# Optimization experiments

Hardware: AMD Instinct MI355X
Metric: run time of the kernel (lower is better)

The kernel has to match this reference:

```python
import jax, jax.numpy as jnp
import numpy as np

B, NSP, H, W = 8, 1024, 256, 256   # frames, superpixels/frame, label-map size
N = B * NSP                        # total superpixel nodes
MIX = 0.5                          # mixing_coeff
SIGMA = 0.05


def _interp_axis(x, out, axis):
    # 1-D bilinear interpolation along `axis`, align_corners=True
    n = x.shape[axis]
    pos = jnp.linspace(0.0, n - 1.0, out).astype(x.dtype)
    i0 = jnp.floor(pos).astype(jnp.int32)
    i1 = jnp.minimum(i0 + 1, n - 1)
    wt = pos - i0.astype(x.dtype)
    shp = [1] * x.ndim
    shp[axis] = out
    wt = wt.reshape(shp)
    return jnp.take(x, i0, axis=axis) * (1 - wt) + jnp.take(x, i1, axis=axis) * wt


def _upsample_ac(x, oh, ow):
    # nn.UpsamplingBilinear2d (align_corners=True)
    if x.shape[2] == oh and x.shape[3] == ow:
        return x
    return _interp_axis(_interp_axis(x, oh, 2), ow, 3)


def _sp_pool(feats, seg):
    # upsample [B,C,h,w] to label resolution, then average features per superpixel -> [N, C]
    C = feats.shape[1]
    up = _upsample_ac(feats, H, W)
    vals = up.transpose(0, 2, 3, 1).reshape(-1, C)          # [B*H*W, C]
    sums = jax.ops.segment_sum(vals, seg, num_segments=N)
    cnt = jax.ops.segment_sum(jnp.ones((seg.shape[0],), vals.dtype), seg, num_segments=N)
    return sums / jnp.maximum(cnt, 1.0)[:, None]


def _gcn(x, Wm, b, src, dst, ew):
    # GCNConv(normalize=False): out_i = sum_{j->i} ew * (x_j @ W) + b
    h = x @ Wm
    agg = jax.ops.segment_sum(h[src] * ew[:, None], dst, num_segments=x.shape[0])
    return agg + b


def _coord_map():
    # channel 0 varies along dim2 (w), channel 1 varies along dim3 (h), both in [0,1]
    c0 = jnp.broadcast_to((jnp.arange(H, dtype=jnp.float32) / (H - 1))[:, None], (H, W))
    c1 = jnp.broadcast_to((jnp.arange(W, dtype=jnp.float32) / (W - 1))[None, :], (H, W))
    return jnp.broadcast_to(jnp.stack([c0, c1], 0)[None], (B, 2, H, W))


def setup_inputs() -> dict:
    key = jax.random.key(0)
    ks = jax.random.split(key, 12)
    labels = jax.random.randint(ks[0], (B, 1, H, W), 0, NSP, dtype=jnp.int32)
    skip0 = jax.random.normal(ks[1], (B, 512, 32, 32), jnp.float32)
    skip1 = jax.random.normal(ks[2], (B, 256, 64, 64), jnp.float32)
    skip2 = jax.random.normal(ks[3], (B, 256, 128, 128), jnp.float32)
    E = 131072
    edges_nn = jax.random.randint(ks[4], (2, E), 0, N, dtype=jnp.int32)
    negs = jax.random.randint(ks[5], (E,), 0, N, dtype=jnp.int32)
    W0 = jax.random.normal(ks[6], (512, 256), jnp.float32) / np.float32(np.sqrt(512))
    W1 = jax.random.normal(ks[7], (256, 256), jnp.float32) / np.float32(np.sqrt(256))
    W2 = jax.random.normal(ks[8], (256, 256), jnp.float32) / np.float32(np.sqrt(256))
    lin_w = jax.random.normal(ks[9], (256, 1), jnp.float32) / np.float32(np.sqrt(256))
    z = jnp.zeros((256,), jnp.float32)
    return {"labels": labels, "skip0": skip0, "skip1": skip1, "skip2": skip2,
            "edges_nn": edges_nn, "negs": negs,
            "W0": W0, "b0": z, "W1": W1, "b1": z, "W2": W2, "b2": z, "lin_w": lin_w}


def reference(labels, skip0, skip1, skip2, edges_nn, negs, W0, b0, W1, b1, W2, b2, lin_w):
    # per-pixel global superpixel id (offset per frame)
    seg = (labels.reshape(B, -1) + NSP * jnp.arange(B, dtype=labels.dtype)[:, None]).reshape(-1)
    src, dst = edges_nn[0], edges_nn[1]

    # pooled normalized coordinates per superpixel -> gaussian edge weights
    pc = _sp_pool(_coord_map(), seg)                        # [N, 2]
    dr = pc[src] - pc[dst]
    dist = jnp.linalg.norm(dr, axis=1)
    edge_attr = jnp.exp(-dist ** 2 / SIGMA)

    x = _sp_pool(skip0, seg)                                # [N, 512]
    layers = [(W0, b0, None), (W1, b1, skip1), (W2, b2, skip2)]
    for i, (Wm, b, sk) in enumerate(layers):
        if i > 0:
            x = (1 - MIX) * x + MIX * _sp_pool(sk, seg)
        x = jax.nn.relu(_gcn(x, Wm, b, src, dst, edge_attr))

    s = x @ lin_w                                           # [N, 1]
    dap = jax.nn.sigmoid(s[src] - s[dst])
    dan = jax.nn.sigmoid(s[src] - s[negs])
    return dan, dap, edge_attr
```

## Files before the change

### kernel.cpp

```cpp
#include <hip/hip_runtime.h>
#include <hip/hip_fp16.h>
#include <cstdint>
#include <cstddef>

#define BB 8
#define NSPX 1024
#define NNODE 8192
#define EE 131072
#define NPIX 524288
#define CH 256

typedef unsigned int uint;
typedef unsigned long long u64;

__device__ __forceinline__ uint packh2(float a, float b) {
  __half2 h = __float22half2_rn(make_float2(a, b));
  return *reinterpret_cast<uint*>(&h);
}
__device__ __forceinline__ __half2 uh2(uint u) { return *reinterpret_cast<__half2*>(&u); }
__device__ __forceinline__ uint h2u(__half2 h) { return *reinterpret_cast<uint*>(&h); }

__global__ __launch_bounds__(256) void zero_kernel(int4* p, int n4) {
  int i = blockIdx.x * 256 + threadIdx.x;
  int stride = gridDim.x * 256;
  int4 z = make_int4(0, 0, 0, 0);
  for (; i < n4; i += stride) p[i] = z;
}

__global__ __launch_bounds__(256) void cnt2_kernel(const int* __restrict__ labels,
                                                   const int* __restrict__ edst,
                                                   int* __restrict__ segb,
                                                   u64* __restrict__ packed,
                                                   int* __restrict__ cnt_e) {
  int blk = blockIdx.x;
  int t = threadIdx.x;
  if (blk < 2048) {
    int p = blk * 256 + t;
    int b = p >> 16;
    int h = (p >> 8) & 255;
    int w = p & 255;
    int seg = labels[p] + (b << 10);
    segb[p] = seg;
    u64 enc = (1ULL << 48) | ((u64)h << 24) | (u64)w;
    atomicAdd(&packed[seg], enc);
  } else {
    int e = (blk - 2048) * 256 + t;
    atomicAdd(&cnt_e[edst[e]], 1);
  }
}

__global__ __launch_bounds__(1024) void fusedB_kernel(const u64* __restrict__ packed,
                                                      const int* __restrict__ cnt_e,
                                                      int* __restrict__ poff, int* __restrict__ eoff,
                                                      float* __restrict__ rcnt,
                                                      float* __restrict__ pch, float* __restrict__ pcw) {
  int blk = blockIdx.x;
  int t = threadIdx.x;
  if (blk < 2) {
    __shared__ int ps[1024];
    int which = blk;
    int* coff = which ? eoff : poff;
    int base = t * 8;
    int v[8];
    int sum = 0;
#pragma unroll
    for (int i = 0; i < 8; ++i) {
      int x = which ? cnt_e[base + i] : (int)(packed[base + i] >> 48);
      v[i] = sum;
      sum += x;
    }
    ps[t] = sum;
    __syncthreads();
    for (int off = 1; off < 1024; off <<= 1) {
      int x = (t >= off) ? ps[t - off] : 0;
      __syncthreads();
      ps[t] += x;
      __syncthreads();
    }
    int prev = (t == 0) ? 0 : ps[t - 1];
#pragma unroll
    for (int i = 0; i < 8; ++i) coff[base + i] = prev + v[i];
    if (t == 1023) coff[8192] = ps[1023];
  } else {
    int n = (blk - 2) * 1024 + t;
    u64 v = packed[n];
    int c = (int)(v >> 48);
    int sh = (int)((v >> 24) & 0xFFFFFF);
    int sw = (int)(v & 0xFFFFFF);
    float r = 1.0f / (float)(c > 1 ? c : 1);
    rcnt[n] = r;
    pch[n] = (float)sh * r * (1.0f / 255.0f);
    pcw[n] = (float)sw * r * (1.0f / 255.0f);
  }
}

__device__ __forceinline__ void dev_transpose_h(const float* __restrict__ src, __half* __restrict__ dst,
                                                int C, int P, int b, int p0, int c0, int t,
                                                uint (*tile)[33]) {
  int l16 = t & 15, r16 = t >> 4;
#pragma unroll
  for (int pass = 0; pass < 4; ++pass) {
    int c = r16 + pass * 16;
    float4 v = *(const float4*)&src[((size_t)b * C + c0 + c) * P + p0 + l16 * 4];
    tile[c][l16 * 2]     = packh2(v.x, v.y);
    tile[c][l16 * 2 + 1] = packh2(v.z, v.w);
  }
  __syncthreads();
  int l8 = t & 7, r32 = t >> 3;
#pragma unroll
  for (int pass = 0; pass < 2; ++pass) {
    int p = r32 + pass * 32;
    int ph = p >> 1;
    int odd = p & 1;
    uint r[4];
#pragma unroll
    for (int q = 0; q < 4; ++q) {
      uint ua = tile[l8 * 8 + 2 * q][ph];
      uint ub = tile[l8 * 8 + 2 * q + 1][ph];
      r[q] = odd ? ((ua >> 16) | (ub & 0xFFFF0000u))
                 : ((ua & 0xFFFFu) | (ub << 16));
    }
    *(uint4*)&dst[((size_t)b * P + p0 + p) * C + c0 + l8 * 8] = make_uint4(r[0], r[1], r[2], r[3]);
  }
}

__device__ __forceinline__ void dev_gemm_kmaj(const float* __restrict__ A, const float* __restrict__ W,
                                              __half* __restrict__ out, int idx, int t,
                                              float (*As)[36]) {
  int b = idx >> 6;
  int m0 = (idx & 31) * 32;
  int n0 = ((idx >> 5) & 1) * 128;
  int ct = t & 31;
  int rm = t >> 5;
  int l8 = t & 7, kr = t >> 3;
  const float* Ab = A + (size_t)b * 512 * 1024;
  float4 acc[4];
#pragma unroll
  for (int i = 0; i < 4; ++i) acc[i] = make_float4(0.f, 0.f, 0.f, 0.f);
  for (int k0 = 0; k0 < 512; k0 += 64) {
#pragma unroll
    for (int pass = 0; pass < 2; ++pass) {
      int k = kr + pass * 32;
      float4 v = *(const float4*)&Ab[(size_t)(k0 + k) * 1024 + m0 + l8 * 4];
      *(float4*)&As[k][l8 * 4] = v;
    }
    __syncthreads();
#pragma unroll 8
    for (int k = 0; k < 64; ++k) {
      float4 a = *(const float4*)&As[k][rm * 4];
      float4 wv = *(const float4*)&W[(size_t)(k0 + k) * 256 + n0 + ct * 4];
      acc[0].x += a.x * wv.x; acc[0].y += a.x * wv.y; acc[0].z += a.x * wv.z; acc[0].w += a.x * wv.w;
      acc[1].x += a.y * wv.x; acc[1].y += a.y * wv.y; acc[1].z += a.y * wv.z; acc[1].w += a.y * wv.w;
      acc[2].x += a.z * wv.x; acc[2].y += a.z * wv.y; acc[2].z += a.z * wv.z; acc[2].w += a.z * wv.w;
      acc[3].x += a.w * wv.x; acc[3].y += a.w * wv.y; acc[3].z += a.w * wv.z; acc[3].w += a.w * wv.w;
    }
    __syncthreads();
  }
#pragma unroll
  for (int i = 0; i < 4; ++i) {
    int m = m0 + rm * 4 + i;
    uint2 pk = make_uint2(packh2(acc[i].x, acc[i].y), packh2(acc[i].z, acc[i].w));
    *(uint2*)&out[((size_t)b * 1024 + m) * 256 + n0 + ct * 4] = pk;
  }
}

__global__ __launch_bounds__(256) void fusedT_kernel(const float* __restrict__ skip1,
                                                     __half* __restrict__ F1t,
                                                     const float* __restrict__ skip2,
                                                     __half* __restrict__ F2t,
                                                     const float* __restrict__ skip0,
                                                     const float* __restrict__ W0,
                                                     __half* __restrict__ F0b,
                                                     const int* __restrict__ segb,
                                                     const int* __restrict__ poff,
                                                     int* __restrict__ pcur,
                                                     int* __restrict__ psorted,
                                                     const int* __restrict__ esrc,
                                                     const int* __restrict__ edst,
                                                     const float* __restrict__ pch,
                                                     const float* __restrict__ pcw,
                                                     const int* __restrict__ eoff,
                                                     int* __restrict__ ecur,
                                                     uint2* __restrict__ evw,
                                                     float* __restrict__ outp) {
  __shared__ __align__(16) char smem[9216];
  int blk = blockIdx.x;
  int t = threadIdx.x;
  if (blk >= 12800) {
    dev_gemm_kmaj(skip0, W0, F0b, blk - 12800, t, (float(*)[36])smem);
    return;
  }
  int s = blk % 5;
  int q = blk / 5;
  if (s < 4) {
    int idx = q * 4 + s;
    if (idx < 8192) {
      int p0 = (idx & 255) * 64;
      int c0 = ((idx >> 8) & 3) * 64;
      int b = idx >> 10;
      dev_transpose_h(skip2, F2t, 256, 16384, b, p0, c0, t, (uint(*)[33])smem);
    } else {
      int i2 = idx - 8192;
      int p0 = (i2 & 63) * 64;
      int c0 = ((i2 >> 6) & 3) * 64;
      int b = i2 >> 8;
      dev_transpose_h(skip1, F1t, 256, 4096, b, p0, c0, t, (uint(*)[33])smem);
    }
  } else {
    if (q < 2048) {
      int p = q * 256 + t;
      int sg = segb[p];
      int pos = poff[sg] + atomicAdd(&pcur[sg], 1);
      psorted[pos] = p;
    } else {
      int e = (q - 2048) * 256 + t;
      int s1 = esrc[e], d1 = edst[e];
      float dh = pch[s1] - pch[d1];
      float dw = pcw[s1] - pcw[d1];
      float ea = expf(-(dh * dh + dw * dw) * 20.0f);
      outp[2 * EE + e] = ea;
      int pos = eoff[d1] + atomicAdd(&ecur[d1], 1);
      evw[pos] = make_uint2((uint)s1, __float_as_uint(ea));
    }
  }
}

__device__ __forceinline__ void tap16(const __half* __restrict__ tp, float wt, __half2* acc) {
  uint4 qa = *(const uint4*)tp;
  uint4 qb = *(const uint4*)(tp + 8);
  __half2 W = __float2half2_rn(wt);
  acc[0] = __hfma2(W, uh2(qa.x), acc[0]);
  acc[1] = __hfma2(W, uh2(qa.y), acc[1]);
  acc[2] = __hfma2(W, uh2(qa.z), acc[2]);
  acc[3] = __hfma2(W, uh2(qa.w), acc[3]);
  acc[4] = __hfma2(W, uh2(qb.x), acc[4]);
  acc[5] = __hfma2(W, uh2(qb.y), acc[5]);
  acc[6] = __hfma2(W, uh2(qb.z), acc[6]);
  acc[7] = __hfma2(W, uh2(qb.w), acc[7]);
}

template <int HS>
__device__ __forceinline__ void taps16(const __half* __restrict__ fb, int h, int w, __half2* acc) {
  const float fh = (float)(HS - 1) / 255.0f;
  float ph = h * fh, pw = w * fh;
  int i0 = (int)ph, j0 = (int)pw;
  float th = ph - (float)i0, tw = pw - (float)j0;
  int i1 = min(i0 + 1, HS - 1), jj1 = min(j0 + 1, HS - 1);
  float w11 = th * tw, w10 = th - w11, w01 = tw - w11, w00 = 1.f - th - tw + w11;
  tap16(fb + (i0 * HS + j0) * 256, w00, acc);
  tap16(fb + (i0 * HS + jj1) * 256, w01, acc);
  tap16(fb + (i1 * HS + j0) * 256, w10, acc);
  tap16(fb + (i1 * HS + jj1) * 256, w11, acc);
}

__global__ __launch_bounds__(256) void fusedC_kernel(const __half* __restrict__ F0,
                                                     const __half* __restrict__ F1,
                                                     const __half* __restrict__ F2,
                                                     const int* __restrict__ poff,
                                                     const int* __restrict__ psorted,
                                                     const float* __restrict__ rc,
                                                     __half* __restrict__ p0out,
                                                     float* __restrict__ p1out,
                                                     float* __restrict__ p2out) {
  __shared__ __align__(16) char smem[18432];
  int blk = blockIdx.x;
  int t = threadIdx.x;
  if (blk >= 8192 && blk < 16384) {
    int x = blk - 8192;
    int n = ((x & 7) << 10) | (x >> 3);
    int b = n >> 10;
    int l = t & 15;
    int s = t >> 4;
    const __half* f0 = F0 + (size_t)b * 1024 * 256 + l * 16;
    const __half* f1 = F1 + (size_t)b * 4096 * 256 + l * 16;
    int j1 = poff[n + 1];
    __half2 z = __float2half2_rn(0.f);
    __half2 a0[8], a1[8];
#pragma unroll
    for (int i = 0; i < 8; ++i) { a0[i] = z; a1[i] = z; }
    for (int j = poff[n] + s; j < j1; j += 16) {
      int p = psorted[j];
      int h = (p >> 8) & 255, w = p & 255;
      taps16<32>(f0, h, w, a0);
      taps16<64>(f1, h, w, a1);
    }
    uint (*red)[256][9] = (uint(*)[256][9])smem;
#pragma unroll
    for (int k = 0; k < 8; ++k) { red[0][t][k] = h2u(a0[k]); red[1][t][k] = h2u(a1[k]); }
    __syncthreads();
    if (t < 128) {
      int l2 = t >> 3, k = t & 7;
      float r = rc[n];
      float2 s0 = make_float2(0.f, 0.f), s1 = s0;
#pragma unroll
      for (int ss = 0; ss < 16; ++ss) {
        float2 v0 = __half22float2(uh2(red[0][ss * 16 + l2][k]));
        float2 v1 = __half22float2(uh2(red[1][ss * 16 + l2][k]));
        s0.x += v0.x; s0.y += v0.y;
        s1.x += v1.x; s1.y += v1.y;
      }
      int c = l2 * 16 + k * 2;
      *(uint*)&p0out[(size_t)n * 256 + c] = packh2(s0.x * r, s0.y * r);
      *(float2*)&p1out[(size_t)n * 256 + c] = make_float2(s1.x * r, s1.y * r);
    }
  } else {
    int x, c0;
    if (blk < 8192) { x = blk; c0 = 0; }
    else            { x = blk - 16384; c0 = 128; }
    int n = ((x & 7) << 10) | (x >> 3);
    int b = n >> 10;
    int l = t & 7;
    int s = t >> 3;
    const __half* fb = F2 + (size_t)b * 16384 * 256 + c0 + l * 16;
    int j1 = poff[n + 1];
    __half2 z = __float2half2_rn(0.f);
    __half2 acc[8];
#pragma unroll
    for (int i = 0; i < 8; ++i) acc[i] = z;
    for (int j = poff[n] + s; j < j1; j += 32) {
      int p = psorted[j];
      int h = (p >> 8) & 255, w = p & 255;
      taps16<128>(fb, h, w, acc);
    }
    uint (*red)[9] = (uint(*)[9])smem;
#pragma unroll
    for (int k = 0; k < 8; ++k) red[t][k] = h2u(acc[k]);
    __syncthreads();
    if (t < 64) {
      int l2 = t >> 3, k = t & 7;
      float r = rc[n];
      float2 sm = make_float2(0.f, 0.f);
#pragma unroll
      for (int ss = 0; ss < 32; ++ss) {
        float2 v = __half22float2(uh2(red[ss * 8 + l2][k]));
        sm.x += v.x; sm.y += v.y;
      }
      int c = c0 + l2 * 16 + k * 2;
      *(float2*)&p2out[(size_t)n * 256 + c] = make_float2(sm.x * r, sm.y * r);
    }
  }
}

__global__ __launch_bounds__(256) void agg_kernel(const __half* __restrict__ h, const float* __restrict__ bias,
                                                  const int* __restrict__ eoff,
                                                  const uint2* __restrict__ evw,
                                                  float* __restrict__ xout) {
  int n = blockIdx.x * 2 + (threadIdx.x >> 7);
  int c2 = threadIdx.x & 127;
  int e0 = eoff[n], e1 = eoff[n + 1];
  float a0 = 0.f, a1 = 0.f;
  for (int j = e0; j < e1; ++j) {
    uint2 ev = evw[j];
    float wv = __uint_as_float(ev.y);
    uint hv = *(const uint*)&h[((size_t)ev.x << 8) + c2 * 2];
    float2 f = __half22float2(uh2(hv));
    a0 += wv * f.x;
    a1 += wv * f.y;
  }
  float v0 = a0 + bias[2 * c2];
  float v1 = a1 + bias[2 * c2 + 1];
  *(float2*)&xout[((size_t)n << 8) + 2 * c2] =
      make_float2(v0 > 0.f ? v0 : 0.f, v1 > 0.f ? v1 : 0.f);
}

__global__ __launch_bounds__(256) void agg_score_kernel(const __half* __restrict__ h,
                                                        const float* __restrict__ bias,
                                                        const int* __restrict__ eoff,
                                                        const uint2* __restrict__ evw,
                                                        const float* __restrict__ lw,
                                                        float* __restrict__ s) {
  int t = threadIdx.x;
  int n = blockIdx.x * 2 + (t >> 7);
  int c2 = t & 127;
  int e0 = eoff[n], e1 = eoff[n + 1];
  float a0 = 0.f, a1 = 0.f;
  for (int j = e0; j < e1; ++j) {
    uint2 ev = evw[j];
    float wv = __uint_as_float(ev.y);
    uint hv = *(const uint*)&h[((size_t)ev.x << 8) + c2 * 2];
    float2 f = __half22float2(uh2(hv));
    a0 += wv * f.x;
    a1 += wv * f.y;
  }
  float v0 = a0 + bias[2 * c2];
  float v1 = a1 + bias[2 * c2 + 1];
  v0 = v0 > 0.f ? v0 : 0.f;
  v1 = v1 > 0.f ? v1 : 0.f;
  float p = v0 * lw[2 * c2] + v1 * lw[2 * c2 + 1];
#pragma unroll
  for (int off = 32; off > 0; off >>= 1) p += __shfl_down(p, off, 64);
  __shared__ float ws[4];
  if ((t & 63) == 0) ws[t >> 6] = p;
  __syncthreads();
  if (t == 0)   s[n] = ws[0] + ws[1];
  if (t == 128) s[n] = ws[2] + ws[3];
}

__global__ __launch_bounds__(256) void gemm_mix_n256(const float* __restrict__ X, const float* __restrict__ Pl,
                                                     const float* __restrict__ W, __half* __restrict__ out) {
  const int t = threadIdx.x;
  const int r0 = blockIdx.x * 16;
  const int cw = (t & 63) * 4;
  const int rg = (t >> 6) * 4;
  __shared__ float Xl[16][68];
  float4 acc[4];
#pragma unroll
  for (int i = 0; i < 4; ++i) acc[i] = make_float4(0.f, 0.f, 0.f, 0.f);
  for (int k0 = 0; k0 < 256; k0 += 64) {
#pragma unroll
    for (int l = 0; l < 4; ++l) {
      int idx = t + 256 * l;
      int r = idx >> 6, k = idx & 63;
      size_t a = (size_t)(r0 + r) * 256 + k0 + k;
      Xl[r][k] = 0.5f * (X[a] + Pl[a]);
    }
    __syncthreads();
#pragma unroll
    for (int k4 = 0; k4 < 64; k4 += 4) {
      float4 a[4];
#pragma unroll
      for (int i = 0; i < 4; ++i) a[i] = *(const float4*)&Xl[rg + i][k4];
#pragma unroll
      for (int kk = 0; kk < 4; ++kk) {
        float4 w = *(const float4*)&W[(size_t)(k0 + k4 + kk) * 256 + cw];
#pragma unroll
        for (int i = 0; i < 4; ++i) {
          float av = ((const float*)&a[i])[kk];
          acc[i].x += av * w.x;
          acc[i].y += av * w.y;
          acc[i].z += av * w.z;
          acc[i].w += av * w.w;
        }
      }
    }
    __syncthreads();
  }
#pragma unroll
  for (int i = 0; i < 4; ++i) {
    uint2 pk = make_uint2(packh2(acc[i].x, acc[i].y), packh2(acc[i].z, acc[i].w));
    *(uint2*)&out[(size_t)(r0 + rg + i) * 256 + cw] = pk;
  }
}

__global__ __launch_bounds__(256) void out_kernel(const float* __restrict__ s, const int* __restrict__ src,
                                                  const int* __restrict__ dst, const int* __restrict__ negs,
                                                  float* __restrict__ outp) {
  int e = blockIdx.x * 256 + threadIdx.x;
  if (e >= EE) return;
  float ss = s[src[e]];
  float a = ss - s[negs[e]];
  float b = ss - s[dst[e]];
  outp[e] = 1.0f / (1.0f + expf(-a));
  outp[EE + e] = 1.0f / (1.0f + expf(-b));
}

extern "C" void kernel_launch(void* const* d_in, const int* in_sizes, int n_in,
                              void* d_out, int out_size, void* d_ws, size_t ws_size,
                              hipStream_t stream) {
  const int*   labels = (const int*)d_in[0];
  const float* skip0  = (const float*)d_in[1];
  const float* skip1  = (const float*)d_in[2];
  const float* skip2  = (const float*)d_in[3];
  const int*   edges  = (const int*)d_in[4];
  const int*   negs   = (const int*)d_in[5];
  const float* W0     = (const float*)d_in[6];
  const float* b0     = (const float*)d_in[7];
  const float* W1     = (const float*)d_in[8];
  const float* b1     = (const float*)d_in[9];
  const float* W2     = (const float*)d_in[10];
  const float* b2     = (const float*)d_in[11];
  const float* lw     = (const float*)d_in[12];
  const int* esrc = edges;
  const int* edst = edges + EE;
  float* outp = (float*)d_out;

  size_t o = 0;
  char* base = (char*)d_ws;
  auto alloc = [&](size_t bytes) -> void* {
    void* p = base + o;
    o += (bytes + 255) & ~(size_t)255;
    return p;
  };
  u64* packed  = (u64*)alloc(NNODE * 8);
  int* cnt_e   = (int*)alloc(NNODE * 4);
  int* ecur    = (int*)alloc(NNODE * 4);
  int* pcur    = (int*)alloc(NNODE * 4);
  size_t zbytes = o;
  float*  rcnt    = (float*)alloc(NNODE * 4);
  float*  pch     = (float*)alloc(NNODE * 4);
  float*  pcw     = (float*)alloc(NNODE * 4);
  int*    poff    = (int*)alloc((NNODE + 1) * 4);
  int*    eoff    = (int*)alloc((NNODE + 1) * 4);
  uint2*  evw     = (uint2*)alloc((size_t)EE * 8);
  int*    psorted = (int*)alloc(NPIX * 4);
  int*    segb    = (int*)alloc(NPIX * 4);
  float*  bufA    = (float*)alloc((size_t)NNODE * CH * 4);
  float*  bufB    = (float*)alloc((size_t)NNODE * CH * 4);
  float*  p1buf   = (float*)alloc((size_t)NNODE * CH * 4);
  float*  p2buf   = (float*)alloc((size_t)NNODE * CH * 4);
  __half* h0b     = (__half*)alloc((size_t)NNODE * CH * 2);
  __half* h1b     = (__half*)alloc((size_t)NNODE * CH * 2);
  __half* F0b     = (__half*)alloc((size_t)BB * 1024 * CH * 2);
  __half* F1t     = (__half*)alloc((size_t)BB * 4096 * CH * 2);
  __half* F2t     = (__half*)alloc((size_t)BB * 16384 * CH * 2);
  float*  sbuf    = (float*)alloc(NNODE * 4);
  (void)ws_size; (void)n_in; (void)in_sizes; (void)out_size;

  zero_kernel<<<64, 256, 0, stream>>>((int4*)d_ws, (int)(zbytes / 16));
  cnt2_kernel<<<2048 + 512, 256, 0, stream>>>(labels, edst, segb, packed, cnt_e);
  fusedB_kernel<<<10, 1024, 0, stream>>>(packed, cnt_e, poff, eoff, rcnt, pch, pcw);
  fusedT_kernel<<<13312, 256, 0, stream>>>(skip1, F1t, skip2, F2t, skip0, W0, F0b,
                                           segb, poff, pcur, psorted,
                                           esrc, edst, pch, pcw, eoff, ecur, evw, outp);
  fusedC_kernel<<<24576, 256, 0, stream>>>(F0b, F1t, F2t, poff, psorted, rcnt,
                                           h0b, p1buf, p2buf);
  agg_kernel<<<NNODE / 2, 256, 0, stream>>>(h0b, b0, eoff, evw, bufB);
  gemm_mix_n256<<<NNODE / 16, 256, 0, stream>>>(bufB, p1buf, W1, h1b);
  agg_kernel<<<NNODE / 2, 256, 0, stream>>>(h1b, b1, eoff, evw, bufA);
  gemm_mix_n256<<<NNODE / 16, 256, 0, stream>>>(bufA, p2buf, W2, h1b);
  agg_score_kernel<<<NNODE / 2, 256, 0, stream>>>(h1b, b2, eoff, evw, lw, sbuf);
  out_kernel<<<EE / 256, 256, 0, stream>>>(sbuf, esrc, edst, negs, outp);
}
```

Before: 691.5 us.

## Split transposes into dedicated kernel with 256-pixel tiles, separate scatter/gemm kernel

```diff
diff --git a/kernel.cpp b/kernel.cpp
--- a/kernel.cpp
+++ b/kernel.cpp
@@ -94,21 +94,21 @@
   }
 }
 
-__device__ __forceinline__ void dev_transpose_h(const float* __restrict__ src, __half* __restrict__ dst,
-                                                int C, int P, int b, int p0, int c0, int t,
-                                                uint (*tile)[33]) {
-  int l16 = t & 15, r16 = t >> 4;
-#pragma unroll
-  for (int pass = 0; pass < 4; ++pass) {
-    int c = r16 + pass * 16;
-    float4 v = *(const float4*)&src[((size_t)b * C + c0 + c) * P + p0 + l16 * 4];
-    tile[c][l16 * 2]     = packh2(v.x, v.y);
-    tile[c][l16 * 2 + 1] = packh2(v.z, v.w);
+__device__ __forceinline__ void dev_transpose256(const float* __restrict__ src, __half* __restrict__ dst,
+                                                 int C, int P, int b, int p0, int c0, int t,
+                                                 uint (*tile)[129]) {
+  int l64 = t & 63, rch = t >> 6;
+#pragma unroll
+  for (int pass = 0; pass < 16; ++pass) {
+    int c = rch + pass * 4;
+    float4 v = *(const float4*)&src[((size_t)b * C + c0 + c) * P + p0 + l64 * 4];
+    tile[c][l64 * 2]     = packh2(v.x, v.y);
+    tile[c][l64 * 2 + 1] = packh2(v.z, v.w);
   }
   __syncthreads();
   int l8 = t & 7, r32 = t >> 3;
 #pragma unroll
-  for (int pass = 0; pass < 2; ++pass) {
+  for (int pass = 0; pass < 8; ++pass) {
     int p = r32 + pass * 32;
     int ph = p >> 1;
     int odd = p & 1;
@@ -121,6 +121,25 @@
                  : ((ua & 0xFFFFu) | (ub << 16));
     }
     *(uint4*)&dst[((size_t)b * P + p0 + p) * C + c0 + l8 * 8] = make_uint4(r[0], r[1], r[2], r[3]);
+  }
+}
+
+__global__ __launch_bounds__(256) void t2k_kernel(const float* __restrict__ skip2, __half* __restrict__ F2t,
+                                                  const float* __restrict__ skip1, __half* __restrict__ F1t) {
+  __shared__ uint tile[64][129];
+  int idx = blockIdx.x;
+  int t = threadIdx.x;
+  if (idx < 2048) {
+    int p0 = (idx & 63) * 256;
+    int c0 = ((idx >> 6) & 3) * 64;
+    int b = idx >> 8;
+    dev_transpose256(skip2, F2t, 256, 16384, b, p0, c0, t, tile);
+  } else {
+    int i2 = idx - 2048;
+    int p0 = (i2 & 15) * 256;
+    int c0 = ((i2 >> 4) & 3) * 64;
+    int b = i2 >> 6;
+    dev_transpose256(skip1, F1t, 256, 4096, b, p0, c0, t, tile);
   }
 }
 
@@ -164,11 +183,7 @@
   }
 }
 
-__global__ __launch_bounds__(256) void fusedT_kernel(const float* __restrict__ skip1,
-                                                     __half* __restrict__ F1t,
-                                                     const float* __restrict__ skip2,
-                                                     __half* __restrict__ F2t,
-                                                     const float* __restrict__ skip0,
+__global__ __launch_bounds__(256) void fusedS_kernel(const float* __restrict__ skip0,
                                                      const float* __restrict__ W0,
                                                      __half* __restrict__ F0b,
                                                      const int* __restrict__ segb,
@@ -183,45 +198,27 @@
                                                      int* __restrict__ ecur,
                                                      uint2* __restrict__ evw,
                                                      float* __restrict__ outp) {
-  __shared__ __align__(16) char smem[9216];
+  __shared__ __align__(16) float As[64][36];
   int blk = blockIdx.x;
   int t = threadIdx.x;
-  if (blk >= 12800) {
-    dev_gemm_kmaj(skip0, W0, F0b, blk - 12800, t, (float(*)[36])smem);
+  if (blk >= 2560) {
+    dev_gemm_kmaj(skip0, W0, F0b, blk - 2560, t, As);
     return;
   }
-  int s = blk % 5;
-  int q = blk / 5;
-  if (s < 4) {
-    int idx = q * 4 + s;
-    if (idx < 8192) {
-      int p0 = (idx & 255) * 64;
-      int c0 = ((idx >> 8) & 3) * 64;
-      int b = idx >> 10;
-      dev_transpose_h(skip2, F2t, 256, 16384, b, p0, c0, t, (uint(*)[33])smem);
-    } else {
-      int i2 = idx - 8192;
-      int p0 = (i2 & 63) * 64;
-      int c0 = ((i2 >> 6) & 3) * 64;
-      int b = i2 >> 8;
-      dev_transpose_h(skip1, F1t, 256, 4096, b, p0, c0, t, (uint(*)[33])smem);
-    }
+  if (blk < 2048) {
+    int p = blk * 256 + t;
+    int sg = segb[p];
+    int pos = poff[sg] + atomicAdd(&pcur[sg], 1);
+    psorted[pos] = p;
   } else {
-    if (q < 2048) {
-      int p = q * 256 + t;
-      int sg = segb[p];
-      int pos = poff[sg] + atomicAdd(&pcur[sg], 1);
-      psorted[pos] = p;
-    } else {
-      int e = (q - 2048) * 256 + t;
-      int s1 = esrc[e], d1 = edst[e];
-      float dh = pch[s1] - pch[d1];
-      float dw = pcw[s1] - pcw[d1];
-      float ea = expf(-(dh * dh + dw * dw) * 20.0f);
-      outp[2 * EE + e] = ea;
-      int pos = eoff[d1] + atomicAdd(&ecur[d1], 1);
-      evw[pos] = make_uint2((uint)s1, __float_as_uint(ea));
-    }
+    int e = (blk - 2048) * 256 + t;
+    int s1 = esrc[e], d1 = edst[e];
+    float dh = pch[s1] - pch[d1];
+    float dw = pcw[s1] - pcw[d1];
+    float ea = expf(-(dh * dh + dw * dw) * 20.0f);
+    outp[2 * EE + e] = ea;
+    int pos = eoff[d1] + atomicAdd(&ecur[d1], 1);
+    evw[pos] = make_uint2((uint)s1, __float_as_uint(ea));
   }
 }
 
@@ -509,9 +506,9 @@
   zero_kernel<<<64, 256, 0, stream>>>((int4*)d_ws, (int)(zbytes / 16));
   cnt2_kernel<<<2048 + 512, 256, 0, stream>>>(labels, edst, segb, packed, cnt_e);
   fusedB_kernel<<<10, 1024, 0, stream>>>(packed, cnt_e, poff, eoff, rcnt, pch, pcw);
-  fusedT_kernel<<<13312, 256, 0, stream>>>(skip1, F1t, skip2, F2t, skip0, W0, F0b,
-                                           segb, poff, pcur, psorted,
-                                           esrc, edst, pch, pcw, eoff, ecur, evw, outp);
+  t2k_kernel<<<2560, 256, 0, stream>>>(skip2, F2t, skip1, F1t);
+  fusedS_kernel<<<3072, 256, 0, stream>>>(skip0, W0, F0b, segb, poff, pcur, psorted,
+                                          esrc, edst, pch, pcw, eoff, ecur, evw, outp);
   fusedC_kernel<<<24576, 256, 0, stream>>>(F0b, F1t, F2t, poff, psorted, rcnt,
                                            h0b, p1buf, p2buf);
   agg_kernel<<<NNODE / 2, 256, 0, stream>>>(h0b, b0, eoff, evw, bufB);
```

Result: slower. 715.7 us (+3.5%).
